# Kernel optimization log

Measured on AMD Instinct MI355X. Metric: run time of the kernel, lower is better.

Reference implementation:

```python
import jax, jax.numpy as jnp
import numpy as np

B, C_IN, C_OUT, H, W = 16, 256, 256, 64, 64
RANK, ORDER = 16, 2
EPS = 1e-5


def setup_inputs() -> dict:
    key = jax.random.key(0)
    k1, k2, k3 = jax.random.split(key, 3)
    x = jax.random.normal(k1, (B, C_IN, H, W), dtype=jnp.float32)
    # torch init: w_core ~ N(0, 1/(C_in*rank)), w_out ~ N(0, 1/rank)
    w_core = jax.random.normal(k2, (RANK, C_IN, RANK), dtype=jnp.float32) * (1.0 / (C_IN * RANK))
    w_out = jax.random.normal(k3, (RANK, C_OUT, RANK), dtype=jnp.float32) * (1.0 / RANK)
    return {"x": x, "w_core": w_core, "w_out": w_out}


def reference(x, w_core, w_out):
    # Per-pixel tensor-ring 1x1 conv.
    # Original chain for order=2 (share_core):
    #   T = einsum('achw,rck->arhwk', x, w_core)
    #   out = einsum('aebcf,afbcg,gdh->aedbch', T, T, w_out)
    #   y   = einsum('arohwr->aohw', out)   # ring trace over e==h
    # Equivalent: M[a,h,w] is rank x rank; P = M^order; y_d = tr(P @ W_d)
    M = jnp.einsum('achw,rck->ahwrk', x, w_core)  # [B,H,W,r,r]
    P = M
    for _ in range(ORDER - 1):
        P = jnp.einsum('ahwef,ahwfg->ahweg', P, M)
    y = jnp.einsum('ahweg,gde->adhw', P, w_out)  # [B,C_out,H,W]
    # InstanceNorm2d (affine=False, biased variance) + Softsign
    mean = jnp.mean(y, axis=(2, 3), keepdims=True)
    var = jnp.var(y, axis=(2, 3), keepdims=True)
    yn = (y - mean) * jax.lax.rsqrt(var + EPS)
    return yn / (1.0 + jnp.abs(yn))
```

## Files before the change

### kernel.cpp

```cpp
#include <hip/hip_runtime.h>

#define HW 4096
#define NC 256
#define ND 256
#define NB 16

typedef _Float16 half4_t __attribute__((ext_vector_type(4)));
typedef _Float16 half8_t __attribute__((ext_vector_type(8)));
typedef float floatx2 __attribute__((ext_vector_type(2)));
typedef float floatx4 __attribute__((ext_vector_type(4)));

#define MSCALE 64.0f
#define INV_MSCALE2 (1.0f / 4096.0f)
#define EPS_SCALED (1e-5f * 4096.0f * 4096.0f)

__global__ __launch_bounds__(256) void prep_weights(
        const float* __restrict__ w_core, const float* __restrict__ w_out,
        _Float16* __restrict__ W1p, _Float16* __restrict__ W2p,
        float* __restrict__ ssum) {
    int tid = blockIdx.x * 256 + threadIdx.x;
    if (tid < 8192) ssum[tid] = 0.f;
    int l   = tid & 63;
    int rt  = (tid >> 6) & 15;
    int ks  = (tid >> 10) & 7;
    int sel = tid >> 13;
    int row = l & 15, kg = l >> 4;
    half8_t v;
    if (sel == 0) {
        int r = rt, k = row;
#pragma unroll
        for (int j = 0; j < 8; ++j) {
            int c = ks * 32 + kg * 8 + j;
            v[j] = (_Float16)(w_core[r * 4096 + c * 16 + k] * MSCALE);
        }
        *(half8_t*)&W1p[(size_t)((ks * 16 + rt) * 64 + l) * 8] = v;
    } else {
        int d = rt * 16 + row;
#pragma unroll
        for (int j = 0; j < 8; ++j) {
            int eg = ks * 32 + kg * 8 + j, e = eg >> 4, g = eg & 15;
            v[j] = (_Float16)w_out[g * 4096 + d * 16 + e];
        }
        *(half8_t*)&W2p[(size_t)((ks * 16 + rt) * 64 + l) * 8] = v;
    }
}

template<bool F16Y>
__global__ __launch_bounds__(256, 4) void compute_y(
        const float* __restrict__ x, const _Float16* __restrict__ W1p,
        const _Float16* __restrict__ W2p, float* __restrict__ y,
        _Float16* __restrict__ y16, float* __restrict__ ssum,
        float* __restrict__ ssq) {
    __shared__ __align__(16) _Float16 R1[8192];
    __shared__ __align__(16) _Float16 R2[8192];

    const int t = threadIdx.x;
    const int l = t & 63, w = t >> 6;
    const int a = blockIdx.x >> 7;
    const int pixbase = (blockIdx.x & 127) * 32;
    const int row16 = l & 15, kg = l >> 4;
    const float* xa = x + (size_t)a * NC * HW + pixbase;

    {
        const int px = t & 31;
        const int o0 = t >> 5;
#pragma unroll
        for (int q = 0; q < 4; ++q) {
            const int oct = q * 8 + o0;
            half8_t hv;
#pragma unroll
            for (int j = 0; j < 8; ++j)
                hv[j] = (_Float16)xa[(size_t)(oct * 8 + j) * HW + px];
            *(half8_t*)&R1[px * 256 + ((oct ^ (px & 15)) << 3)] = hv;
        }
    }
    __syncthreads();

    floatx4 acc[4][2];
#pragma unroll
    for (int i = 0; i < 4; ++i)
#pragma unroll
        for (int j = 0; j < 2; ++j) acc[i][j] = (floatx4){0.f, 0.f, 0.f, 0.f};
    {
        const half8_t* W1v = (const half8_t*)W1p;
        half8_t af[4], afn[4];
#pragma unroll
        for (int rq = 0; rq < 4; ++rq) af[rq] = W1v[(w * 4 + rq) * 64 + l];
        for (int ks = 0; ks < 8; ++ks) {
            if (ks < 7) {
#pragma unroll
                for (int rq = 0; rq < 4; ++rq)
                    afn[rq] = W1v[((ks + 1) * 16 + w * 4 + rq) * 64 + l];
            }
#pragma unroll
            for (int pt = 0; pt < 2; ++pt) {
                const int px = pt * 16 + row16;
                half8_t bf = *(const half8_t*)
                    &R1[px * 256 + (((ks * 4 + kg) ^ row16) << 3)];
#pragma unroll
                for (int rq = 0; rq < 4; ++rq)
                    acc[rq][pt] = __builtin_amdgcn_mfma_f32_16x16x32_f16(
                                      af[rq], bf, acc[rq][pt], 0, 0, 0);
            }
#pragma unroll
            for (int rq = 0; rq < 4; ++rq) af[rq] = afn[rq];
        }
    }
#pragma unroll
    for (int rq = 0; rq < 4; ++rq) {
        const int rk4 = (w * 4 + rq) * 4 + kg;
#pragma unroll
        for (int pt = 0; pt < 2; ++pt) {
            const int px = pt * 16 + row16;
            half4_t hv;
#pragma unroll
            for (int r2 = 0; r2 < 4; ++r2) hv[r2] = (_Float16)acc[rq][pt][r2];
            *(half4_t*)&R2[px * 256 + ((rk4 ^ row16) << 2)] = hv;
        }
    }
    __syncthreads();

    const half8_t* W2v = (const half8_t*)W2p;
    half8_t caf[4], cafn[4];
#pragma unroll
    for (int dq = 0; dq < 4; ++dq) caf[dq] = W2v[(w * 4 + dq) * 64 + l];

    {
        const int p = t >> 3, qe = t & 7, ps = p & 15;
        const _Float16* Mp = &R2[p * 256];
        float Af[2][16];
#pragma unroll
        for (int i = 0; i < 2; ++i) {
            const int e = i * 8 + qe;
#pragma unroll
            for (int f4 = 0; f4 < 4; ++f4) {
                half4_t v = *(const half4_t*)
                    &Mp[(((e * 4 + f4) ^ ps) << 2)];
#pragma unroll
                for (int j = 0; j < 4; ++j) Af[i][f4 * 4 + j] = (float)v[j];
            }
        }
        floatx2 Pacc[2][8];
#pragma unroll
        for (int i = 0; i < 2; ++i)
#pragma unroll
            for (int g2 = 0; g2 < 8; ++g2) Pacc[i][g2] = (floatx2){0.f, 0.f};
#pragma unroll
        for (int f = 0; f < 16; ++f) {
            floatx2 Bg[8];
#pragma unroll
            for (int g4 = 0; g4 < 4; ++g4) {
                half4_t v = *(const half4_t*)
                    &Mp[(((f * 4 + g4) ^ ps) << 2)];
                Bg[g4 * 2]     = (floatx2){(float)v[0], (float)v[1]};
                Bg[g4 * 2 + 1] = (floatx2){(float)v[2], (float)v[3]};
            }
#pragma unroll
            for (int i = 0; i < 2; ++i) {
                floatx2 a2 = {Af[i][f], Af[i][f]};
#pragma unroll
                for (int g2 = 0; g2 < 8; ++g2)
                    Pacc[i][g2] = __builtin_elementwise_fma(a2, Bg[g2], Pacc[i][g2]);
            }
        }
#pragma unroll
        for (int i = 0; i < 2; ++i) {
            const int e = i * 8 + qe;
#pragma unroll
            for (int h2 = 0; h2 < 2; ++h2) {
                half8_t hv;
#pragma unroll
                for (int j = 0; j < 8; ++j)
                    hv[j] = (_Float16)Pacc[i][h2 * 4 + (j >> 1)][j & 1];
                *(half8_t*)&R1[p * 256 + (((e * 2 + h2) ^ ps) << 3)] = hv;
            }
        }
    }
    __syncthreads();

    floatx4 cacc[4][2];
#pragma unroll
    for (int i = 0; i < 4; ++i)
#pragma unroll
        for (int j = 0; j < 2; ++j) cacc[i][j] = (floatx4){0.f, 0.f, 0.f, 0.f};
    for (int ks = 0; ks < 8; ++ks) {
        if (ks < 7) {
#pragma unroll
            for (int dq = 0; dq < 4; ++dq)
                cafn[dq] = W2v[((ks + 1) * 16 + w * 4 + dq) * 64 + l];
        }
#pragma unroll
        for (int pt = 0; pt < 2; ++pt) {
            const int px = pt * 16 + row16;
            half8_t bf = *(const half8_t*)
                &R1[px * 256 + (((ks * 4 + kg) ^ row16) << 3)];
#pragma unroll
            for (int dq = 0; dq < 4; ++dq)
                cacc[dq][pt] = __builtin_amdgcn_mfma_f32_16x16x32_f16(
                                   caf[dq], bf, cacc[dq][pt], 0, 0, 0);
        }
#pragma unroll
        for (int dq = 0; dq < 4; ++dq) caf[dq] = cafn[dq];
    }

    float*     ya   = y   + (size_t)a * ND * HW + pixbase;
    _Float16*  ya16 = F16Y ? (y16 + (size_t)a * ND * HW + pixbase) : nullptr;
#pragma unroll
    for (int dq = 0; dq < 4; ++dq) {
        const int dbase = (w * 4 + dq) * 16 + kg * 4;
#pragma unroll
        for (int r2 = 0; r2 < 4; ++r2) {
            const int d = dbase + r2;
            float s = 0.f, q2 = 0.f;
#pragma unroll
            for (int pt = 0; pt < 2; ++pt) {
                float v;
                if (F16Y) {
                    _Float16 hv = (_Float16)cacc[dq][pt][r2];
                    ya16[(size_t)d * HW + pt * 16 + row16] = hv;
                    v = (float)hv;
                } else {
                    v = cacc[dq][pt][r2] * INV_MSCALE2;
                    ya[(size_t)d * HW + pt * 16 + row16] = v;
                }
                s += v; q2 += v * v;
            }
#pragma unroll
            for (int off = 1; off < 16; off <<= 1) {
                s  += __shfl_xor(s, off);
                q2 += __shfl_xor(q2, off);
            }
            if (row16 == 0) {
                atomicAdd(&ssum[a * 256 + d], s);
                atomicAdd(&ssq [a * 256 + d], q2);
            }
        }
    }
}

__global__ __launch_bounds__(256) void finalize_f16(
        const _Float16* __restrict__ y16, const float* __restrict__ ssum,
        const float* __restrict__ ssq, float* __restrict__ out) {
    const int ad = blockIdx.x;
    const float m  = ssum[ad] * (1.f / HW);
    const float sv = ssq[ad] * (1.f / HW) - m * m;
    const float s  = rsqrtf(sv + EPS_SCALED);
    const size_t base = (size_t)ad * HW + threadIdx.x * 16;
    half8_t h0 = *(const half8_t*)&y16[base];
    half8_t h1 = *(const half8_t*)&y16[base + 8];
    float o[16];
#pragma unroll
    for (int j = 0; j < 8; ++j) {
        float z0 = ((float)h0[j] - m) * s;
        float z1 = ((float)h1[j] - m) * s;
        o[j]     = z0 / (1.f + fabsf(z0));
        o[8 + j] = z1 / (1.f + fabsf(z1));
    }
#pragma unroll
    for (int q = 0; q < 4; ++q)
        *(float4*)&out[base + q * 4] =
            make_float4(o[q * 4], o[q * 4 + 1], o[q * 4 + 2], o[q * 4 + 3]);
}

__global__ __launch_bounds__(256) void finalize_f32(
        float* __restrict__ y, const float* __restrict__ ssum,
        const float* __restrict__ ssq) {
    const int i4 = blockIdx.x * 256 + threadIdx.x;
    const int ad = i4 >> 10;
    const float m  = ssum[ad] * (1.f / HW);
    const float sv = ssq[ad] * (1.f / HW) - m * m;
    const float s  = rsqrtf(sv + 1e-5f);
    float4 v = ((const float4*)y)[i4];
    float vv[4] = {v.x, v.y, v.z, v.w};
#pragma unroll
    for (int lq = 0; lq < 4; ++lq) {
        float z = (vv[lq] - m) * s;
        vv[lq] = z / (1.f + fabsf(z));
    }
    ((float4*)y)[i4] = make_float4(vv[0], vv[1], vv[2], vv[3]);
}

extern "C" void kernel_launch(void* const* d_in, const int* in_sizes, int n_in,
                              void* d_out, int out_size, void* d_ws, size_t ws_size,
                              hipStream_t stream) {
    const float* x      = (const float*)d_in[0];
    const float* w_core = (const float*)d_in[1];
    const float* w_out  = (const float*)d_in[2];
    float* y = (float*)d_out;

    char* wsb = (char*)d_ws;
    _Float16* W1p = (_Float16*)wsb;
    _Float16* W2p = (_Float16*)(wsb + 131072);
    float* ssum   = (float*)(wsb + 262144);
    float* ssq    = (float*)(wsb + 278528);
    _Float16* y16 = (_Float16*)(wsb + 294912);

    const size_t need_f16 = 294912 + (size_t)NB * ND * HW * sizeof(_Float16);
    const bool use_f16 = ws_size >= need_f16;

    prep_weights<<<64, 256, 0, stream>>>(w_core, w_out, W1p, W2p, ssum);
    if (use_f16) {
        compute_y<true><<<2048, 256, 0, stream>>>(x, W1p, W2p, y, y16, ssum, ssq);
        finalize_f16<<<4096, 256, 0, stream>>>(y16, ssum, ssq, y);
    } else {
        compute_y<false><<<2048, 256, 0, stream>>>(x, W1p, W2p, y, nullptr, ssum, ssq);
        finalize_f32<<<16384, 256, 0, stream>>>(y, ssum, ssq);
    }
}
```

Measured before the change: 100.7 us.

## Double pixel tile per block and keep M in fp32 shared memory

Each block now handles 64 pixels instead of 32, halving the grid and doubling MFMA tiles per wave so weight fragments are reused across more pixels. The intermediate M matrix is stored in fp32 in a single aliased 64KB shared buffer instead of fp16, which avoids conversions and extra rounding. P is converted with packed RTZ conversions. Occupancy drops to 2 blocks per CU and register pressure grows, which may reduce latency hiding.

New measurement: 82.50 us. -18.1%, faster.

```diff
diff --git a/kernel.cpp b/kernel.cpp
--- a/kernel.cpp
+++ b/kernel.cpp
@@ -5,8 +5,10 @@
 #define ND 256
 #define NB 16
 
+typedef _Float16 half2_t __attribute__((ext_vector_type(2)));
 typedef _Float16 half4_t __attribute__((ext_vector_type(4)));
 typedef _Float16 half8_t __attribute__((ext_vector_type(8)));
+typedef __fp16   fp16x2  __attribute__((ext_vector_type(2)));
 typedef float floatx2 __attribute__((ext_vector_type(2)));
 typedef float floatx4 __attribute__((ext_vector_type(4)));
 
@@ -46,41 +48,43 @@
 }
 
 template<bool F16Y>
-__global__ __launch_bounds__(256, 4) void compute_y(
+__global__ __launch_bounds__(256, 2) void compute_y(
         const float* __restrict__ x, const _Float16* __restrict__ W1p,
         const _Float16* __restrict__ W2p, float* __restrict__ y,
         _Float16* __restrict__ y16, float* __restrict__ ssum,
         float* __restrict__ ssq) {
-    __shared__ __align__(16) _Float16 R1[8192];
-    __shared__ __align__(16) _Float16 R2[8192];
+    __shared__ __align__(16) float S[16384];
+    _Float16* XT  = (_Float16*)S;
+    float*    Mf  = S;
+    _Float16* PLb = (_Float16*)S;
 
     const int t = threadIdx.x;
     const int l = t & 63, w = t >> 6;
-    const int a = blockIdx.x >> 7;
-    const int pixbase = (blockIdx.x & 127) * 32;
+    const int a = blockIdx.x >> 6;
+    const int pixbase = (blockIdx.x & 63) * 64;
     const int row16 = l & 15, kg = l >> 4;
     const float* xa = x + (size_t)a * NC * HW + pixbase;
 
     {
-        const int px = t & 31;
-        const int o0 = t >> 5;
-#pragma unroll
-        for (int q = 0; q < 4; ++q) {
-            const int oct = q * 8 + o0;
+        const int px = t & 63;
+        const int o0 = t >> 6;
+#pragma unroll
+        for (int q = 0; q < 8; ++q) {
+            const int oct = q * 4 + o0;
             half8_t hv;
 #pragma unroll
             for (int j = 0; j < 8; ++j)
                 hv[j] = (_Float16)xa[(size_t)(oct * 8 + j) * HW + px];
-            *(half8_t*)&R1[px * 256 + ((oct ^ (px & 15)) << 3)] = hv;
+            *(half8_t*)&XT[px * 256 + ((oct ^ (px & 15)) << 3)] = hv;
         }
     }
     __syncthreads();
 
-    floatx4 acc[4][2];
+    floatx4 acc[4][4];
 #pragma unroll
     for (int i = 0; i < 4; ++i)
 #pragma unroll
-        for (int j = 0; j < 2; ++j) acc[i][j] = (floatx4){0.f, 0.f, 0.f, 0.f};
+        for (int j = 0; j < 4; ++j) acc[i][j] = (floatx4){0.f, 0.f, 0.f, 0.f};
     {
         const half8_t* W1v = (const half8_t*)W1p;
         half8_t af[4], afn[4];
@@ -93,10 +97,10 @@
                     afn[rq] = W1v[((ks + 1) * 16 + w * 4 + rq) * 64 + l];
             }
 #pragma unroll
-            for (int pt = 0; pt < 2; ++pt) {
+            for (int pt = 0; pt < 4; ++pt) {
                 const int px = pt * 16 + row16;
                 half8_t bf = *(const half8_t*)
-                    &R1[px * 256 + (((ks * 4 + kg) ^ row16) << 3)];
+                    &XT[px * 256 + (((ks * 4 + kg) ^ row16) << 3)];
 #pragma unroll
                 for (int rq = 0; rq < 4; ++rq)
                     acc[rq][pt] = __builtin_amdgcn_mfma_f32_16x16x32_f16(
@@ -106,43 +110,42 @@
             for (int rq = 0; rq < 4; ++rq) af[rq] = afn[rq];
         }
     }
-#pragma unroll
-    for (int rq = 0; rq < 4; ++rq) {
-        const int rk4 = (w * 4 + rq) * 4 + kg;
-#pragma unroll
-        for (int pt = 0; pt < 2; ++pt) {
-            const int px = pt * 16 + row16;
-            half4_t hv;
-#pragma unroll
-            for (int r2 = 0; r2 < 4; ++r2) hv[r2] = (_Float16)acc[rq][pt][r2];
-            *(half4_t*)&R2[px * 256 + ((rk4 ^ row16) << 2)] = hv;
-        }
-    }
-    __syncthreads();
 
     const half8_t* W2v = (const half8_t*)W2p;
     half8_t caf[4], cafn[4];
 #pragma unroll
     for (int dq = 0; dq < 4; ++dq) caf[dq] = W2v[(w * 4 + dq) * 64 + l];
 
+    __syncthreads();
+
+#pragma unroll
+    for (int rq = 0; rq < 4; ++rq) {
+        const int u = (w * 4 + rq) * 4 + kg;
+#pragma unroll
+        for (int pt = 0; pt < 4; ++pt) {
+            const int px = pt * 16 + row16;
+            *(floatx4*)&Mf[px * 256 + ((u ^ row16) << 2)] = acc[rq][pt];
+        }
+    }
+    __syncthreads();
+
     {
-        const int p = t >> 3, qe = t & 7, ps = p & 15;
-        const _Float16* Mp = &R2[p * 256];
-        float Af[2][16];
-#pragma unroll
-        for (int i = 0; i < 2; ++i) {
-            const int e = i * 8 + qe;
+        const int p = t >> 2, qe = t & 3, ps = p & 15;
+        const float* Mp = &Mf[p * 256];
+        float Af[4][16];
+#pragma unroll
+        for (int i = 0; i < 4; ++i) {
+            const int e = i * 4 + qe;
 #pragma unroll
             for (int f4 = 0; f4 < 4; ++f4) {
-                half4_t v = *(const half4_t*)
-                    &Mp[(((e * 4 + f4) ^ ps) << 2)];
-#pragma unroll
-                for (int j = 0; j < 4; ++j) Af[i][f4 * 4 + j] = (float)v[j];
-            }
-        }
-        floatx2 Pacc[2][8];
-#pragma unroll
-        for (int i = 0; i < 2; ++i)
+                floatx4 v = *(const floatx4*)&Mp[(((e * 4 + f4) ^ ps) << 2)];
+#pragma unroll
+                for (int j = 0; j < 4; ++j) Af[i][f4 * 4 + j] = v[j];
+            }
+        }
+        floatx2 Pacc[4][8];
+#pragma unroll
+        for (int i = 0; i < 4; ++i)
 #pragma unroll
             for (int g2 = 0; g2 < 8; ++g2) Pacc[i][g2] = (floatx2){0.f, 0.f};
 #pragma unroll
@@ -150,13 +153,12 @@
             floatx2 Bg[8];
 #pragma unroll
             for (int g4 = 0; g4 < 4; ++g4) {
-                half4_t v = *(const half4_t*)
-                    &Mp[(((f * 4 + g4) ^ ps) << 2)];
-                Bg[g4 * 2]     = (floatx2){(float)v[0], (float)v[1]};
-                Bg[g4 * 2 + 1] = (floatx2){(float)v[2], (float)v[3]};
-            }
-#pragma unroll
-            for (int i = 0; i < 2; ++i) {
+                floatx4 v = *(const floatx4*)&Mp[(((f * 4 + g4) ^ ps) << 2)];
+                Bg[g4 * 2]     = (floatx2){v[0], v[1]};
+                Bg[g4 * 2 + 1] = (floatx2){v[2], v[3]};
+            }
+#pragma unroll
+            for (int i = 0; i < 4; ++i) {
                 floatx2 a2 = {Af[i][f], Af[i][f]};
 #pragma unroll
                 for (int g2 = 0; g2 < 8; ++g2)
@@ -164,25 +166,29 @@
             }
         }
 #pragma unroll
-        for (int i = 0; i < 2; ++i) {
-            const int e = i * 8 + qe;
+        for (int i = 0; i < 4; ++i) {
+            const int e = i * 4 + qe;
 #pragma unroll
             for (int h2 = 0; h2 < 2; ++h2) {
                 half8_t hv;
 #pragma unroll
-                for (int j = 0; j < 8; ++j)
-                    hv[j] = (_Float16)Pacc[i][h2 * 4 + (j >> 1)][j & 1];
-                *(half8_t*)&R1[p * 256 + (((e * 2 + h2) ^ ps) << 3)] = hv;
+                for (int g2 = 0; g2 < 4; ++g2) {
+                    fp16x2 pk = __builtin_amdgcn_cvt_pkrtz(
+                        Pacc[i][h2 * 4 + g2][0], Pacc[i][h2 * 4 + g2][1]);
+                    hv[g2 * 2]     = (_Float16)pk[0];
+                    hv[g2 * 2 + 1] = (_Float16)pk[1];
+                }
+                *(half8_t*)&PLb[p * 512 + (((e * 2 + h2) ^ ps) << 3)] = hv;
             }
         }
     }
     __syncthreads();
 
-    floatx4 cacc[4][2];
+    floatx4 cacc[4][4];
 #pragma unroll
     for (int i = 0; i < 4; ++i)
 #pragma unroll
-        for (int j = 0; j < 2; ++j) cacc[i][j] = (floatx4){0.f, 0.f, 0.f, 0.f};
+        for (int j = 0; j < 4; ++j) cacc[i][j] = (floatx4){0.f, 0.f, 0.f, 0.f};
     for (int ks = 0; ks < 8; ++ks) {
         if (ks < 7) {
 #pragma unroll
@@ -190,10 +196,10 @@
                 cafn[dq] = W2v[((ks + 1) * 16 + w * 4 + dq) * 64 + l];
         }
 #pragma unroll
-        for (int pt = 0; pt < 2; ++pt) {
+        for (int pt = 0; pt < 4; ++pt) {
             const int px = pt * 16 + row16;
             half8_t bf = *(const half8_t*)
-                &R1[px * 256 + (((ks * 4 + kg) ^ row16) << 3)];
+                &PLb[px * 512 + (((ks * 4 + kg) ^ row16) << 3)];
 #pragma unroll
             for (int dq = 0; dq < 4; ++dq)
                 cacc[dq][pt] = __builtin_amdgcn_mfma_f32_16x16x32_f16(
@@ -213,7 +219,7 @@
             const int d = dbase + r2;
             float s = 0.f, q2 = 0.f;
 #pragma unroll
-            for (int pt = 0; pt < 2; ++pt) {
+            for (int pt = 0; pt < 4; ++pt) {
                 float v;
                 if (F16Y) {
                     _Float16 hv = (_Float16)cacc[dq][pt][r2];
@@ -300,10 +306,10 @@
 
     prep_weights<<<64, 256, 0, stream>>>(w_core, w_out, W1p, W2p, ssum);
     if (use_f16) {
-        compute_y<true><<<2048, 256, 0, stream>>>(x, W1p, W2p, y, y16, ssum, ssq);
+        compute_y<true><<<1024, 256, 0, stream>>>(x, W1p, W2p, y, y16, ssum, ssq);
         finalize_f16<<<4096, 256, 0, stream>>>(y16, ssum, ssq, y);
     } else {
-        compute_y<false><<<2048, 256, 0, stream>>>(x, W1p, W2p, y, nullptr, ssum, ssq);
+        compute_y<false><<<1024, 256, 0, stream>>>(x, W1p, W2p, y, nullptr, ssum, ssq);
         finalize_f32<<<16384, 256, 0, stream>>>(y, ssum, ssq);
     }
 }
```
